# Performance work log

Measured on AMD Instinct MI355X. Metric: run time of the kernel, lower is better.

## Reference

```python
import jax, jax.numpy as jnp
import numpy as np

N = 50000       # nodes
E = 800000      # edges (avg degree 16)
IN_DIM = 64
H = 64          # hidden_dim
OUT_DIM = 64
R = 8           # n_relations
L = 3           # n_layers
LN_EPS = 1e-5
NEG_SLOPE = 0.2


def _layer_norm(x, g, b):
    mu = jnp.mean(x, axis=-1, keepdims=True)
    var = jnp.mean((x - mu) ** 2, axis=-1, keepdims=True)
    return (x - mu) * jax.lax.rsqrt(var + LN_EPS) * g + b


def setup_inputs() -> dict:
    key = jax.random.key(0)
    ks = jax.random.split(key, 10)
    s = 0.05
    return {
        "x": jax.random.normal(ks[0], (N, IN_DIM), jnp.float32),
        "edge_index": jax.random.randint(ks[1], (2, E), 0, N),
        "edge_type": jax.random.randint(ks[2], (E,), 0, R),
        "W_in": jax.random.normal(ks[3], (H, IN_DIM), jnp.float32) * s,
        "b_in": jnp.zeros((H,), jnp.float32),
        "W_rel": jax.random.normal(ks[4], (R, H, H), jnp.float32) * s,   # no bias
        "W_gate": jax.random.normal(ks[5], (R, H, H), jnp.float32) * s,
        "b_gate": jnp.zeros((R, H), jnp.float32),
        "W_att": jax.random.normal(ks[6], (R, 2 * H), jnp.float32) * s,  # Linear(2H,1) per relation
        "b_att": jnp.zeros((R,), jnp.float32),
        "ln_gamma": jnp.ones((L, H), jnp.float32),
        "ln_beta": jnp.zeros((L, H), jnp.float32),
        "W_out": jax.random.normal(ks[7], (OUT_DIM, H), jnp.float32) * s,
        "b_out": jnp.zeros((OUT_DIM,), jnp.float32),
    }


def reference(x, edge_index, edge_type, W_in, b_in, W_rel, W_gate, b_gate,
              W_att, b_att, ln_gamma, ln_beta, W_out, b_out):
    src, dst = edge_index[0], edge_index[1]
    Wa_src, Wa_dst = W_att[:, :H], W_att[:, H:]      # [R,H] each
    seg = dst * R + edge_type                        # combined (node, relation) scatter key
    eidx = jnp.arange(E)

    h = jax.nn.relu(x @ W_in.T + b_in)               # [N,H]

    for layer in range(L):
        h_src = h[src]                               # [E,H] gather
        h_dst = h[dst]                               # [E,H] gather
        # attention score of each edge under its own relation's Linear(2H,1)
        scores_all = h_src @ Wa_src.T + h_dst @ Wa_dst.T + b_att   # [E,R]
        scores = scores_all[eidx, edge_type]                        # [E]
        scores = jax.nn.leaky_relu(scores, NEG_SLOPE)
        # softmax over dim=0 within each relation's edge set (as in the torch code)
        m = jax.ops.segment_max(scores, edge_type, num_segments=R)
        ex = jnp.exp(scores - m[edge_type])
        denom = jax.ops.segment_sum(ex, edge_type, num_segments=R)
        att = ex / denom[edge_type]                                 # [E]
        # relation-specific linear of source features (linear commutes with gather)
        hWr = jnp.einsum('nh,rkh->nrk', h, W_rel)                   # [N,R,H]
        msg = hWr[src, edge_type] * att[:, None]                    # [E,H]
        # per-relation scatter-add into destinations
        agg = jax.ops.segment_sum(msg, seg, num_segments=N * R)     # [N*R,H]
        agg = agg.reshape(N, R, H)
        gate = jax.nn.sigmoid(jnp.einsum('nh,rkh->nrk', h, W_gate) + b_gate)  # [N,R,H]
        h_new = jnp.mean(gate * agg, axis=1)         # sum(messages)/n_relations
        h = jax.nn.relu(_layer_norm(h + h_new, ln_gamma[layer], ln_beta[layer]))

    return h @ W_out.T + b_out
```

## Files before the change

kernel.cpp:

```cpp
#include <hip/hip_runtime.h>
#include <math.h>

#define NN 50000
#define EE 800000
#define HH 64
#define RR 8
#define LL 3
#define NR (NN * RR)
#define NB ((NR + 255) / 256)
#define LN_EPS 1e-5f
#define NEG_SLOPE 0.2f
#define LDH 68
#define PNB 584
#define OTB (16 * LDH)
#define DSPREAD 64

typedef __attribute__((ext_vector_type(8))) short bf8;
typedef __attribute__((ext_vector_type(4))) float f4;
typedef __attribute__((ext_vector_type(8))) unsigned short us8;
typedef __attribute__((ext_vector_type(2))) unsigned int u2;

__device__ __forceinline__ unsigned short bf16r(float f) {
    unsigned u = __float_as_uint(f);
    unsigned r = u + 0x7fffu + ((u >> 16) & 1u);
    return (unsigned short)(r >> 16);
}
__device__ __forceinline__ float bf2f(unsigned short u) {
    return __uint_as_float(((unsigned)u) << 16);
}

__global__ void proj_in(const float* __restrict__ x, const float* __restrict__ W,
                        const float* __restrict__ bias, const float* __restrict__ W_att,
                        float* __restrict__ h, unsigned short* __restrict__ hbf,
                        float* __restrict__ s_src, float* __restrict__ s_dst) {
    __shared__ float WT[64 * 65];
    __shared__ float xs[4 * 64];
    int tid = threadIdx.x;
    #pragma unroll
    for (int s = 0; s < 16; ++s) {
        int idx = tid + 256 * s;
        int k = idx >> 6, i = idx & 63;
        WT[i * 65 + k] = W[idx];
    }
    int w = tid >> 6, l = tid & 63;
    int n = blockIdx.x * 4 + w;
    xs[w * 64 + l] = x[(size_t)n * 64 + l];
    __syncthreads();
    float acc = 0.f;
    #pragma unroll
    for (int i = 0; i < 64; ++i) acc += xs[w * 64 + i] * WT[i * 65 + l];
    acc += bias[l];
    acc = fmaxf(acc, 0.f);
    h[(size_t)n * 64 + l] = acc;
    hbf[(size_t)n * 64 + l] = bf16r(acc);
    float wsrc[8], wdst[8];
    #pragma unroll
    for (int r = 0; r < 8; ++r) {
        wsrc[r] = W_att[r * 128 + l];
        wdst[r] = W_att[r * 128 + 64 + l];
    }
    #pragma unroll
    for (int r = 0; r < 8; ++r) {
        float v = acc * wsrc[r];
        float u = acc * wdst[r];
        #pragma unroll
        for (int off = 1; off <= 32; off <<= 1) {
            v += __shfl_xor(v, off, 64);
            u += __shfl_xor(u, off, 64);
        }
        if (l == r) s_src[n * 8 + r] = v;
        if (l == 8 + r) s_dst[n * 8 + r] = u;
    }
}

__global__ void edge_count(const int* __restrict__ ei, const int* __restrict__ et,
                           int* __restrict__ counts, int* __restrict__ rank) {
    int e = blockIdx.x * 256 + threadIdx.x;
    int d = ei[EE + e], t = et[e];
    rank[e] = atomicAdd(&counts[d * 8 + t], 1);
}

__global__ void scan1(const int* __restrict__ counts, int* __restrict__ offs,
                      int* __restrict__ bsum) {
    __shared__ int s[256];
    int tid = threadIdx.x;
    int i = blockIdx.x * 256 + tid;
    int v = (i < NR) ? counts[i] : 0;
    s[tid] = v; __syncthreads();
    for (int d = 1; d < 256; d <<= 1) {
        int x = (tid >= d) ? s[tid - d] : 0;
        __syncthreads();
        s[tid] += x;
        __syncthreads();
    }
    if (i < NR) offs[i] = s[tid] - v;
    if (tid == 255) bsum[blockIdx.x] = s[255];
}

__global__ void scan2(int* __restrict__ bsum) {
    __shared__ int s[1024];
    int tid = threadIdx.x;
    int carry = 0;
    for (int c0 = 0; c0 < NB; c0 += 1024) {
        int i = c0 + tid;
        int v = (i < NB) ? bsum[i] : 0;
        s[tid] = v; __syncthreads();
        for (int d = 1; d < 1024; d <<= 1) {
            int x = (tid >= d) ? s[tid - d] : 0;
            __syncthreads();
            s[tid] += x;
            __syncthreads();
        }
        if (i < NB) bsum[i] = carry + s[tid] - v;
        int tot = s[1023];
        __syncthreads();
        carry += tot;
    }
}

__global__ void edge_fill(const int* __restrict__ ei, const int* __restrict__ et,
                          const int* __restrict__ rank, const int* __restrict__ offs,
                          const int* __restrict__ bsum, u2* __restrict__ spack) {
    int e = blockIdx.x * 256 + threadIdx.x;
    int s = ei[e], d = ei[EE + e], t = et[e];
    int seg = d * 8 + t;
    int slot = offs[seg] + bsum[seg >> 8] + rank[e];
    spack[slot] = (u2){(unsigned)s, (unsigned)seg};
}

__global__ void cvt_w(const float* __restrict__ Wr, const float* __restrict__ Wg,
                      const float* __restrict__ Wa, const float* __restrict__ Wo,
                      unsigned short* __restrict__ WrB, unsigned short* __restrict__ WgB,
                      unsigned short* __restrict__ WaB, unsigned short* __restrict__ WoB) {
    int i = blockIdx.x * 256 + threadIdx.x;
    WrB[i] = bf16r(Wr[i]);
    WgB[i] = bf16r(Wg[i]);
    if (i < 1024) {
        int row = i >> 6, k = i & 63;
        float v = (row < 8) ? Wa[row * 128 + k] : Wa[(row - 8) * 128 + 64 + k];
        WaB[i] = bf16r(v);
    }
    if (i < 4096) WoB[i] = bf16r(Wo[i]);
}

__global__ void edge_softmax2(const u2* __restrict__ spack,
                              const float* __restrict__ s_src, const float* __restrict__ s_dst,
                              const float* __restrict__ b_att,
                              u2* __restrict__ epack, float* __restrict__ dpart) {
    __shared__ float lsum[4][8];
    int tid = threadIdx.x;
    if (tid < 32) lsum[tid >> 3][tid & 7] = 0.f;
    __syncthreads();
    int slot = blockIdx.x * 256 + tid;
    u2 sp = spack[slot];
    int src = (int)sp[0];
    int seg = (int)sp[1];
    int t = seg & 7;
    float sc = s_src[src * 8 + t] + s_dst[seg] + b_att[t];
    sc = (sc >= 0.f) ? sc : NEG_SLOPE * sc;
    float ex = __expf(sc);
    epack[slot] = (u2){(unsigned)src, __float_as_uint(ex)};
    atomicAdd(&lsum[tid >> 6][t], ex);
    __syncthreads();
    if (tid < 8) {
        float v = lsum[0][tid] + lsum[1][tid] + lsum[2][tid] + lsum[3][tid];
        atomicAdd(&dpart[(blockIdx.x & (DSPREAD - 1)) * 16 + tid], v);
    }
}

template<bool EMIT, bool OUT>
__global__ __launch_bounds__(256, 8) void combine_fused(
    const float* __restrict__ hbuf, const unsigned short* __restrict__ hbf_in,
    const int* __restrict__ offs, const int* __restrict__ bsum,
    const u2* __restrict__ epack, const float* __restrict__ dpartL,
    const unsigned short* __restrict__ WrB, const unsigned short* __restrict__ WgB,
    const unsigned short* __restrict__ WaB, const unsigned short* __restrict__ WoB,
    const float* __restrict__ b_gate, const float* __restrict__ gamma,
    const float* __restrict__ beta, float* __restrict__ hout,
    unsigned short* __restrict__ hbf_out, float* __restrict__ ssrc_out,
    float* __restrict__ sdst_out, float* __restrict__ outp,
    const float* __restrict__ b_out) {
    __shared__ float hs[16 * LDH];
    __shared__ alignas(16) unsigned short ps[16 * PNB];
    __shared__ float idn8[8];
    __shared__ int offsL[129];
    float* ps_f = (float*)ps;
    int tid = threadIdx.x;
    int n0 = blockIdx.x * 16;

    {
        int row = tid >> 4, c4 = tid & 15;
        f4 v = ((const f4*)hbuf)[(size_t)(n0 + row) * 16 + c4];
        *(f4*)&hs[row * LDH + c4 * 4] = v;
    }
    if (tid < 129) {
        int sidx = n0 * 8 + tid;
        offsL[tid] = (sidx < NR) ? (offs[sidx] + bsum[sidx >> 8]) : EE;
    }
    if (tid < 64) {
        int t = tid & 7, g = tid >> 3;
        float sm = 0.f;
        #pragma unroll
        for (int j = 0; j < 8; ++j) sm += dpartL[(g * 8 + j) * 16 + t];
        sm += __shfl_xor(sm, 8, 64);
        sm += __shfl_xor(sm, 16, 64);
        sm += __shfl_xor(sm, 32, 64);
        if (tid < 8) idn8[t] = 1.f / sm;
    }
    __syncthreads();

    {
        int segl = tid >> 1;
        int half = tid & 1;
        int lo = offsL[segl], hi = offsL[segl + 1];
        int r = segl & 7;
        int gn = segl >> 3;
        float fa[32];
        #pragma unroll
        for (int j = 0; j < 32; ++j) fa[j] = 0.f;
        for (int s = lo; s < hi; s += 2) {
            u2 pk0 = epack[s];
            int s1 = (s + 1 < hi) ? (s + 1) : s;
            u2 pk1 = epack[s1];
            float a0 = __uint_as_float(pk0[1]);
            float a1 = (s + 1 < hi) ? __uint_as_float(pk1[1]) : 0.f;
            const us8* hp0 = (const us8*)(hbf_in + ((size_t)(int)pk0[0] << 6) + half * 32);
            const us8* hp1 = (const us8*)(hbf_in + ((size_t)(int)pk1[0] << 6) + half * 32);
            #pragma unroll
            for (int q = 0; q < 4; ++q) {
                us8 v0 = hp0[q];
                us8 v1 = hp1[q];
                #pragma unroll
                for (int j = 0; j < 8; ++j) {
                    fa[q * 8 + j] += a0 * bf2f(v0[j]);
                    fa[q * 8 + j] += a1 * bf2f(v1[j]);
                }
            }
        }
        float sA = idn8[r];
        unsigned short* pp = &ps[gn * PNB + r * 72 + half * 32];
        #pragma unroll
        for (int q = 0; q < 4; ++q) {
            us8 o;
            #pragma unroll
            for (int j = 0; j < 8; ++j) o[j] = bf16r(fa[q * 8 + j] * sA);
            *(us8*)(pp + q * 8) = o;
        }
    }
    __syncthreads();

    int w = tid >> 6, lane = tid & 63;
    int quad = lane >> 4, lr = lane & 15;
    int tn = w;

    bf8 a_h[2];
    #pragma unroll
    for (int kb = 0; kb < 2; ++kb) {
        const float* p = &hs[lr * LDH + kb * 32 + quad * 8];
        bf8 a;
        #pragma unroll
        for (int j = 0; j < 8; ++j) a[j] = (short)bf16r(p[j]);
        a_h[kb] = a;
    }

    f4 acc = (f4){0.f, 0.f, 0.f, 0.f};
    for (int r = 0; r < 8; ++r) {
        bf8 a_p[2];
        #pragma unroll
        for (int kb = 0; kb < 2; ++kb)
            a_p[kb] = *(const bf8*)&ps[lr * PNB + r * 72 + kb * 32 + quad * 8];
        f4 aggc = (f4){0.f, 0.f, 0.f, 0.f};
        f4 gacc = (f4){0.f, 0.f, 0.f, 0.f};
        #pragma unroll
        for (int kb = 0; kb < 2; ++kb) {
            const bf8* br = (const bf8*)(WrB + ((r * 64 + tn * 16 + lr) * 64 + kb * 32 + quad * 8));
            const bf8* bg = (const bf8*)(WgB + ((r * 64 + tn * 16 + lr) * 64 + kb * 32 + quad * 8));
            aggc = __builtin_amdgcn_mfma_f32_16x16x32_bf16(a_p[kb], *br, aggc, 0, 0, 0);
            gacc = __builtin_amdgcn_mfma_f32_16x16x32_bf16(a_h[kb], *bg, gacc, 0, 0, 0);
        }
        float bg = b_gate[r * 64 + tn * 16 + lr];
        #pragma unroll
        for (int j = 0; j < 4; ++j) {
            float g = 1.f / (1.f + __expf(-(gacc[j] + bg)));
            acc[j] += g * aggc[j];
        }
    }
    __syncthreads();

    #pragma unroll
    for (int j = 0; j < 4; ++j) {
        int row = quad * 4 + j;
        int col = tn * 16 + lr;
        ps_f[row * LDH + col] = hs[row * LDH + col] + acc[j] * 0.125f;
    }
    __syncthreads();

    {
        int row = tid >> 4, c = tid & 15;
        int n = n0 + row;
        f4 tv = *(const f4*)&ps_f[row * LDH + c * 4];
        float s1 = tv[0] + tv[1] + tv[2] + tv[3];
        float s2 = tv[0]*tv[0] + tv[1]*tv[1] + tv[2]*tv[2] + tv[3]*tv[3];
        #pragma unroll
        for (int off = 1; off <= 8; off <<= 1) {
            s1 += __shfl_xor(s1, off, 64);
            s2 += __shfl_xor(s2, off, 64);
        }
        float mu = s1 * (1.f / 64.f);
        float var = s2 * (1.f / 64.f) - mu * mu;
        float rs = rsqrtf(var + LN_EPS);
        f4 g = *(const f4*)(gamma + c * 4);
        f4 b = *(const f4*)(beta + c * 4);
        f4 ov;
        #pragma unroll
        for (int j = 0; j < 4; ++j)
            ov[j] = fmaxf((tv[j] - mu) * rs * g[j] + b[j], 0.f);
        if (!OUT)
            *(f4*)(hout + (size_t)n * 64 + c * 4) = ov;
        *(f4*)&ps_f[OTB + row * LDH + c * 4] = ov;
        if (EMIT) {
            u2 u;
            u[0] = (unsigned)bf16r(ov[0]) | ((unsigned)bf16r(ov[1]) << 16);
            u[1] = (unsigned)bf16r(ov[2]) | ((unsigned)bf16r(ov[3]) << 16);
            *(u2*)(hbf_out + (size_t)n * 64 + c * 4) = u;
        }
    }

    if (EMIT) {
        __syncthreads();
        if (w == 0) {
            f4 sc = (f4){0.f, 0.f, 0.f, 0.f};
            #pragma unroll
            for (int kb = 0; kb < 2; ++kb) {
                const float* p = &ps_f[OTB + lr * LDH + kb * 32 + quad * 8];
                bf8 a;
                #pragma unroll
                for (int j = 0; j < 8; ++j) a[j] = (short)bf16r(p[j]);
                const bf8* bw = (const bf8*)(WaB + lr * 64 + kb * 32 + quad * 8);
                sc = __builtin_amdgcn_mfma_f32_16x16x32_bf16(a, *bw, sc, 0, 0, 0);
            }
            #pragma unroll
            for (int j = 0; j < 4; ++j) {
                int n = n0 + quad * 4 + j;
                if (lr < 8) ssrc_out[n * 8 + lr] = sc[j];
                else        sdst_out[n * 8 + (lr - 8)] = sc[j];
            }
        }
    }

    if (OUT) {
        __syncthreads();
        f4 oc = (f4){0.f, 0.f, 0.f, 0.f};
        #pragma unroll
        for (int kb = 0; kb < 2; ++kb) {
            const float* p = &ps_f[OTB + lr * LDH + kb * 32 + quad * 8];
            bf8 a;
            #pragma unroll
            for (int j = 0; j < 8; ++j) a[j] = (short)bf16r(p[j]);
            const bf8* bw = (const bf8*)(WoB + ((tn * 16 + lr) * 64 + kb * 32 + quad * 8));
            oc = __builtin_amdgcn_mfma_f32_16x16x32_bf16(a, *bw, oc, 0, 0, 0);
        }
        float bo = b_out[tn * 16 + lr];
        #pragma unroll
        for (int j = 0; j < 4; ++j)
            outp[(size_t)(n0 + quad * 4 + j) * 64 + tn * 16 + lr] = oc[j] + bo;
    }
}

extern "C" void kernel_launch(void* const* d_in, const int* in_sizes, int n_in,
                              void* d_out, int out_size, void* d_ws, size_t ws_size,
                              hipStream_t stream) {
    const float* x      = (const float*)d_in[0];
    const int*   ei     = (const int*)d_in[1];
    const int*   et     = (const int*)d_in[2];
    const float* W_in   = (const float*)d_in[3];
    const float* b_in   = (const float*)d_in[4];
    const float* W_rel  = (const float*)d_in[5];
    const float* W_gate = (const float*)d_in[6];
    const float* b_gate = (const float*)d_in[7];
    const float* W_att  = (const float*)d_in[8];
    const float* b_att  = (const float*)d_in[9];
    const float* ln_g   = (const float*)d_in[10];
    const float* ln_b   = (const float*)d_in[11];
    const float* W_out  = (const float*)d_in[12];
    const float* b_out  = (const float*)d_in[13];
    float* out = (float*)d_out;

    float* h0 = (float*)d_out;

    char* ws = (char*)d_ws;
    float* h1 = (float*)ws;                     ws += (size_t)NN * 64 * 4;
    unsigned short* hbfA = (unsigned short*)ws; ws += (size_t)NN * 64 * 2;
    unsigned short* hbfB = (unsigned short*)ws; ws += (size_t)NN * 64 * 2;
    float* s_src = (float*)ws;                  ws += (size_t)NN * 8 * 4;
    float* s_dst = (float*)ws;                  ws += (size_t)NN * 8 * 4;
    unsigned short* WrB = (unsigned short*)ws;  ws += (size_t)RR * 64 * 64 * 2;
    unsigned short* WgB = (unsigned short*)ws;  ws += (size_t)RR * 64 * 64 * 2;
    unsigned short* WaB = (unsigned short*)ws;  ws += 2048;
    unsigned short* WoB = (unsigned short*)ws;  ws += 8192;
    int* counts = (int*)ws;                     ws += (size_t)NR * 4;
    float* dpart = (float*)ws;                  ws += 3 * DSPREAD * 16 * 4;
    int* offs = (int*)ws;                       ws += (size_t)NR * 4;
    int* bsum = (int*)ws;                       ws += 6400;
    int* rank = (int*)ws;                       ws += (size_t)EE * 4;
    u2* spack = (u2*)ws;                        ws += (size_t)EE * 8;
    u2* epack = (u2*)ws;                        ws += (size_t)EE * 8;

    hipMemsetAsync(counts, 0, (size_t)NR * 4 + 3 * DSPREAD * 16 * 4, stream);
    cvt_w<<<128, 256, 0, stream>>>(W_rel, W_gate, W_att, W_out, WrB, WgB, WaB, WoB);
    edge_count<<<EE / 256, 256, 0, stream>>>(ei, et, counts, rank);
    scan1<<<NB, 256, 0, stream>>>(counts, offs, bsum);
    scan2<<<1, 1024, 0, stream>>>(bsum);
    edge_fill<<<EE / 256, 256, 0, stream>>>(ei, et, rank, offs, bsum, spack);
    proj_in<<<NN / 4, 256, 0, stream>>>(x, W_in, b_in, W_att, h0, hbfA, s_src, s_dst);

    const int tiles16 = NN / 16;
    float* hA = h0;  float* hB = h1;
    unsigned short* bfA = hbfA;  unsigned short* bfB = hbfB;
    for (int layer = 0; layer < LL; ++layer) {
        float* dpl = dpart + (size_t)layer * DSPREAD * 16;
        edge_softmax2<<<EE / 256, 256, 0, stream>>>(spack, s_src, s_dst, b_att,
                                                    epack, dpl);
        if (layer < LL - 1) {
            combine_fused<true, false><<<tiles16, 256, 0, stream>>>(
                hA, bfA, offs, bsum, epack, dpl, WrB, WgB, WaB, WoB, b_gate,
                ln_g + layer * 64, ln_b + layer * 64,
                hB, bfB, s_src, s_dst, out, b_out);
        } else {
            combine_fused<false, true><<<tiles16, 256, 0, stream>>>(
                hA, bfA, offs, bsum, epack, dpl, WrB, WgB, WaB, WoB, b_gate,
                ln_g + layer * 64, ln_b + layer * 64,
                hB, bfB, s_src, s_dst, out, b_out);
        }
        float* tf = hA; hA = hB; hB = tf;
        unsigned short* tb = bfA; bfA = bfB; bfB = tb;
    }
}
```

Baseline: 468.2 us.

## Retile input projection to 16 nodes per block and drop combine's fp32 h staging

```diff
diff --git a/kernel.cpp b/kernel.cpp
--- a/kernel.cpp
+++ b/kernel.cpp
@@ -29,47 +29,71 @@
     return __uint_as_float(((unsigned)u) << 16);
 }
 
-__global__ void proj_in(const float* __restrict__ x, const float* __restrict__ W,
-                        const float* __restrict__ bias, const float* __restrict__ W_att,
-                        float* __restrict__ h, unsigned short* __restrict__ hbf,
-                        float* __restrict__ s_src, float* __restrict__ s_dst) {
-    __shared__ float WT[64 * 65];
-    __shared__ float xs[4 * 64];
+__global__ __launch_bounds__(256) void proj_in(
+    const float* __restrict__ x, const float* __restrict__ W,
+    const float* __restrict__ bias, const unsigned short* __restrict__ WaB,
+    float* __restrict__ h, unsigned short* __restrict__ hbf,
+    float* __restrict__ s_src, float* __restrict__ s_dst) {
+    __shared__ float WT[64 * LDH];
+    __shared__ float xs[16 * LDH];
+    __shared__ float hs[16 * LDH];
     int tid = threadIdx.x;
+    int n0 = blockIdx.x * 16;
     #pragma unroll
     for (int s = 0; s < 16; ++s) {
         int idx = tid + 256 * s;
         int k = idx >> 6, i = idx & 63;
-        WT[i * 65 + k] = W[idx];
-    }
-    int w = tid >> 6, l = tid & 63;
-    int n = blockIdx.x * 4 + w;
-    xs[w * 64 + l] = x[(size_t)n * 64 + l];
-    __syncthreads();
-    float acc = 0.f;
-    #pragma unroll
-    for (int i = 0; i < 64; ++i) acc += xs[w * 64 + i] * WT[i * 65 + l];
-    acc += bias[l];
-    acc = fmaxf(acc, 0.f);
-    h[(size_t)n * 64 + l] = acc;
-    hbf[(size_t)n * 64 + l] = bf16r(acc);
-    float wsrc[8], wdst[8];
-    #pragma unroll
-    for (int r = 0; r < 8; ++r) {
-        wsrc[r] = W_att[r * 128 + l];
-        wdst[r] = W_att[r * 128 + 64 + l];
-    }
-    #pragma unroll
-    for (int r = 0; r < 8; ++r) {
-        float v = acc * wsrc[r];
-        float u = acc * wdst[r];
-        #pragma unroll
-        for (int off = 1; off <= 32; off <<= 1) {
-            v += __shfl_xor(v, off, 64);
-            u += __shfl_xor(u, off, 64);
-        }
-        if (l == r) s_src[n * 8 + r] = v;
-        if (l == 8 + r) s_dst[n * 8 + r] = u;
+        WT[i * LDH + k] = W[idx];
+    }
+    int row = tid >> 4, cg = tid & 15;
+    {
+        f4 v = ((const f4*)x)[(size_t)(n0 + row) * 16 + cg];
+        *(f4*)&xs[row * LDH + cg * 4] = v;
+    }
+    __syncthreads();
+    f4 acc;
+    {
+        f4 b = *(const f4*)(bias + cg * 4);
+        acc = b;
+        #pragma unroll
+        for (int i = 0; i < 64; ++i) {
+            float xv = xs[row * LDH + i];
+            f4 wt = *(const f4*)&WT[i * LDH + cg * 4];
+            acc[0] += xv * wt[0];
+            acc[1] += xv * wt[1];
+            acc[2] += xv * wt[2];
+            acc[3] += xv * wt[3];
+        }
+        #pragma unroll
+        for (int j = 0; j < 4; ++j) acc[j] = fmaxf(acc[j], 0.f);
+        int n = n0 + row;
+        *(f4*)(h + (size_t)n * 64 + cg * 4) = acc;
+        u2 u;
+        u[0] = (unsigned)bf16r(acc[0]) | ((unsigned)bf16r(acc[1]) << 16);
+        u[1] = (unsigned)bf16r(acc[2]) | ((unsigned)bf16r(acc[3]) << 16);
+        *(u2*)(hbf + (size_t)n * 64 + cg * 4) = u;
+        *(f4*)&hs[row * LDH + cg * 4] = acc;
+    }
+    __syncthreads();
+    if (tid < 64) {
+        int lane = tid;
+        int quad = lane >> 4, lr = lane & 15;
+        f4 sc = (f4){0.f, 0.f, 0.f, 0.f};
+        #pragma unroll
+        for (int kb = 0; kb < 2; ++kb) {
+            const float* p = &hs[lr * LDH + kb * 32 + quad * 8];
+            bf8 a;
+            #pragma unroll
+            for (int j = 0; j < 8; ++j) a[j] = (short)bf16r(p[j]);
+            const bf8* bw = (const bf8*)(WaB + lr * 64 + kb * 32 + quad * 8);
+            sc = __builtin_amdgcn_mfma_f32_16x16x32_bf16(a, *bw, sc, 0, 0, 0);
+        }
+        #pragma unroll
+        for (int j = 0; j < 4; ++j) {
+            int n = n0 + quad * 4 + j;
+            if (lr < 8) s_src[n * 8 + lr] = sc[j];
+            else        s_dst[n * 8 + (lr - 8)] = sc[j];
+        }
     }
 }
 
@@ -180,7 +204,6 @@
     unsigned short* __restrict__ hbf_out, float* __restrict__ ssrc_out,
     float* __restrict__ sdst_out, float* __restrict__ outp,
     const float* __restrict__ b_out) {
-    __shared__ float hs[16 * LDH];
     __shared__ alignas(16) unsigned short ps[16 * PNB];
     __shared__ float idn8[8];
     __shared__ int offsL[129];
@@ -188,24 +211,19 @@
     int tid = threadIdx.x;
     int n0 = blockIdx.x * 16;
 
-    {
-        int row = tid >> 4, c4 = tid & 15;
-        f4 v = ((const f4*)hbuf)[(size_t)(n0 + row) * 16 + c4];
-        *(f4*)&hs[row * LDH + c4 * 4] = v;
-    }
     if (tid < 129) {
         int sidx = n0 * 8 + tid;
         offsL[tid] = (sidx < NR) ? (offs[sidx] + bsum[sidx >> 8]) : EE;
     }
-    if (tid < 64) {
-        int t = tid & 7, g = tid >> 3;
+    if (tid >= 192) {
+        int t = tid & 7, g = (tid - 192) >> 3;
         float sm = 0.f;
         #pragma unroll
         for (int j = 0; j < 8; ++j) sm += dpartL[(g * 8 + j) * 16 + t];
         sm += __shfl_xor(sm, 8, 64);
         sm += __shfl_xor(sm, 16, 64);
         sm += __shfl_xor(sm, 32, 64);
-        if (tid < 8) idn8[t] = 1.f / sm;
+        if ((tid & 63) < 8) idn8[t] = 1.f / sm;
     }
     __syncthreads();
 
@@ -255,13 +273,8 @@
 
     bf8 a_h[2];
     #pragma unroll
-    for (int kb = 0; kb < 2; ++kb) {
-        const float* p = &hs[lr * LDH + kb * 32 + quad * 8];
-        bf8 a;
-        #pragma unroll
-        for (int j = 0; j < 8; ++j) a[j] = (short)bf16r(p[j]);
-        a_h[kb] = a;
-    }
+    for (int kb = 0; kb < 2; ++kb)
+        a_h[kb] = *(const bf8*)(hbf_in + ((size_t)(n0 + lr) << 6) + kb * 32 + quad * 8);
 
     f4 acc = (f4){0.f, 0.f, 0.f, 0.f};
     for (int r = 0; r < 8; ++r) {
@@ -291,7 +304,7 @@
     for (int j = 0; j < 4; ++j) {
         int row = quad * 4 + j;
         int col = tn * 16 + lr;
-        ps_f[row * LDH + col] = hs[row * LDH + col] + acc[j] * 0.125f;
+        ps_f[row * LDH + col] = hbuf[(size_t)(n0 + row) * 64 + col] + acc[j] * 0.125f;
     }
     __syncthreads();
 
@@ -317,6 +330,7 @@
             ov[j] = fmaxf((tv[j] - mu) * rs * g[j] + b[j], 0.f);
         if (!OUT)
             *(f4*)(hout + (size_t)n * 64 + c * 4) = ov;
+        __syncthreads();
         *(f4*)&ps_f[OTB + row * LDH + c * 4] = ov;
         if (EMIT) {
             u2 u;
@@ -412,7 +426,7 @@
     scan1<<<NB, 256, 0, stream>>>(counts, offs, bsum);
     scan2<<<1, 1024, 0, stream>>>(bsum);
     edge_fill<<<EE / 256, 256, 0, stream>>>(ei, et, rank, offs, bsum, spack);
-    proj_in<<<NN / 4, 256, 0, stream>>>(x, W_in, b_in, W_att, h0, hbfA, s_src, s_dst);
+    proj_in<<<NN / 16, 256, 0, stream>>>(x, W_in, b_in, WaB, h0, hbfA, s_src, s_dst);
 
     const int tiles16 = NN / 16;
     float* hA = h0;  float* hB = h1;
```

Result: faster. 424.8 us (-9.3%).
